# Kernel tuning notes

Hardware: AMD Instinct MI355X
Metric: run time of the kernel (lower is better)

## Reference

```python
import jax, jax.numpy as jnp
import numpy as np

N, E = 50000, 800000
IN_F, OUT_F, EMB, KER = 64, 64, 3, 4


def setup_inputs() -> dict:
    key = jax.random.key(0)
    ks = jax.random.split(key, 6)
    x = jax.random.normal(ks[0], (N, IN_F), dtype=jnp.float32)
    edge_idx = jax.random.randint(ks[1], (2, E), 0, N, dtype=jnp.int64)
    spec_domain = jax.random.normal(ks[2], (N, EMB), dtype=jnp.float32)
    weight = 0.1 * jax.random.normal(ks[3], (IN_F, OUT_F, KER), dtype=jnp.float32)
    bias_p = 0.1 * jax.random.normal(ks[4], (OUT_F,), dtype=jnp.float32)
    mu = 0.005 * jax.random.normal(ks[5], (EMB, KER), dtype=jnp.float32)
    sig = jnp.ones((1, KER), dtype=jnp.float32)  # repo default 60140 underflows exp with random embeddings
    return {"x": x, "edge_idx": edge_idx, "spec_domain": spec_domain,
            "weight": weight, "bias_p": bias_p, "mu": mu, "sig": sig}


def reference(x, edge_idx, spec_domain, weight, bias_p, mu, sig):
    n = x.shape[0]
    row, col = edge_idx[0], edge_idx[1]
    # support for all kernels at once: [N, out, K]
    support = jnp.einsum('ni,iok->nok', x, weight)
    # per-edge Gaussian kernel values: [E, K]
    diff = spec_domain[row] - spec_domain[col]               # [E, emb]
    dm = diff[:, :, None] - mu[None, :, :]                   # [E, emb, K]
    qq = -0.5 * jnp.sum(dm * dm, axis=1)                     # [E, K]
    value = jnp.exp(sig[0][None, :] * qq)                    # [E, K]
    # sparse mm: out[row] += value * support[col], per kernel
    msgs = value[:, None, :] * support[col]                  # [E, out, K]
    out = jax.ops.segment_sum(msgs, row, num_segments=n)     # [N, out, K]
    return out.sum(axis=2) + bias_p
```

## Files before the change

### kernel.cpp

```cpp
#include <hip/hip_runtime.h>
#include <hip/hip_fp16.h>

#define FIN 64
#define CAP 48
#define BINSH 8
#define NBINMAX 256
#define PCAP 5120
#define TILE_B 4096

typedef __attribute__((ext_vector_type(8))) short short8v;
typedef __attribute__((ext_vector_type(4))) float f32x4v;

__device__ __forceinline__ unsigned pk_bf16(float a, float b) {
    unsigned ua = __builtin_bit_cast(unsigned, a);
    unsigned ub = __builtin_bit_cast(unsigned, b);
    ua = (ua + 0x7FFFu + ((ua >> 16) & 1u)) >> 16;
    ub = (ub + 0x7FFFu + ((ub >> 16) & 1u)) >> 16;
    return ua | (ub << 16);
}

__global__ __launch_bounds__(256) void p1_kernel(const float* __restrict__ x,
                                                 const float* __restrict__ weight,
                                                 __half* __restrict__ sup,
                                                 const int* __restrict__ eidx,
                                                 int* __restrict__ gcur,
                                                 int* __restrict__ part,
                                                 int n, int e_total, int sblocks) {
    const int t = threadIdx.x;
    __shared__ unsigned short xb[32][72];
    __shared__ int hist[NBINMAX], lbase[NBINMAX], gbase[NBINMAX];
    __shared__ int wsum[4];

    const int rowbase = blockIdx.x * 32;
    if (rowbase < n) {
        {
            int nrows = n - rowbase; if (nrows > 32) nrows = 32;
            int nf2 = nrows * 32;
            const float2* __restrict__ x2 = (const float2*)(x + (size_t)rowbase * 64);
            #pragma unroll
            for (int j = 0; j < 4; ++j) {
                int idx = t + j * 256;
                if (idx < nf2) {
                    float2 v = x2[idx];
                    int r = idx >> 5, c2 = idx & 31;
                    *(unsigned*)&xb[r][c2 * 2] = pk_bf16(v.x, v.y);
                }
            }
        }
        __syncthreads();

        const int lane = t & 63;
        const int w4 = t >> 6;
        const int lm = lane & 15, lg = lane >> 4;

        short8v a[2][2];
        #pragma unroll
        for (int mt = 0; mt < 2; ++mt)
            #pragma unroll
            for (int kb = 0; kb < 2; ++kb)
                a[mt][kb] = *(const short8v*)&xb[mt * 16 + lm][kb * 32 + lg * 8];

        f32x4v acc[2][4];
        #pragma unroll
        for (int mt = 0; mt < 2; ++mt)
            #pragma unroll
            for (int nt = 0; nt < 4; ++nt)
                acc[mt][nt] = (f32x4v){0.f, 0.f, 0.f, 0.f};

        #pragma unroll
        for (int nt = 0; nt < 4; ++nt) {
            const int col = (w4 * 4 + nt) * 16 + lm;
            short8v bfr[2];
            #pragma unroll
            for (int kb = 0; kb < 2; ++kb) {
                short8v bb;
                #pragma unroll
                for (int j = 0; j < 8; ++j) {
                    float wv = weight[(kb * 32 + lg * 8 + j) * 256 + col];
                    unsigned u = __builtin_bit_cast(unsigned, wv);
                    bb[j] = (short)((u + 0x7FFFu + ((u >> 16) & 1u)) >> 16);
                }
                bfr[kb] = bb;
            }
            #pragma unroll
            for (int mt = 0; mt < 2; ++mt) {
                acc[mt][nt] = __builtin_amdgcn_mfma_f32_16x16x32_bf16(a[mt][0], bfr[0], acc[mt][nt], 0, 0, 0);
                acc[mt][nt] = __builtin_amdgcn_mfma_f32_16x16x32_bf16(a[mt][1], bfr[1], acc[mt][nt], 0, 0, 0);
            }
        }

        #pragma unroll
        for (int mt = 0; mt < 2; ++mt) {
            const int row0 = rowbase + mt * 16 + lg * 4;
            #pragma unroll
            for (int reg = 0; reg < 4; ++reg) {
                if (row0 + reg < n) {
                    #pragma unroll
                    for (int nt = 0; nt < 4; ++nt) {
                        int col = (w4 * 4 + nt) * 16 + lm;
                        sup[(size_t)(row0 + reg) * 256 + col] = __float2half(acc[mt][nt][reg]);
                    }
                }
            }
        }
    }

    if (blockIdx.x < sblocks) {
        int nz = 0;
        #pragma unroll
        for (int j = 1; j < 16; j += 2) nz |= eidx[j];
        const int is64 = (nz == 0);

        hist[t] = 0;
        __syncthreads();

        const int base = blockIdx.x * TILE_B;
        int nv = e_total - base;
        if (nv > TILE_B) nv = TILE_B;
        if (nv < 0) nv = 0;

        int pay[16], bn[16], lp[16];
        #pragma unroll
        for (int i = 0; i < 8; ++i) {
            const int pl = t + 256 * i;
            const int pg = (base >> 1) + pl;
            int r0 = 0, c0 = 0, r1 = 0, c1 = 0, v0 = 0, v1 = 0;
            if (2 * pl < nv) {
                if (is64) {
                    int4 rr = ((const int4*)eidx)[pg];
                    int4 cc = ((const int4*)(eidx + 2 * (size_t)e_total))[pg];
                    r0 = rr.x; c0 = cc.x; v0 = 1;
                    if (2 * pl + 1 < nv) { r1 = rr.z; c1 = cc.z; v1 = 1; }
                } else {
                    int2 rr = ((const int2*)eidx)[pg];
                    int2 cc = ((const int2*)(eidx + (size_t)e_total))[pg];
                    r0 = rr.x; c0 = cc.x; v0 = 1;
                    if (2 * pl + 1 < nv) { r1 = rr.y; c1 = cc.y; v1 = 1; }
                }
            }
            pay[2 * i]     = (c0 << 8) | (r0 & 255);
            bn[2 * i]      = v0 ? (r0 >> BINSH) : -1;
            pay[2 * i + 1] = (c1 << 8) | (r1 & 255);
            bn[2 * i + 1]  = v1 ? (r1 >> BINSH) : -1;
        }
        #pragma unroll
        for (int i = 0; i < 16; ++i) {
            lp[i] = (bn[i] >= 0) ? atomicAdd(&hist[bn[i]], 1) : 0;
        }
        __syncthreads();

        {
            const int lane = t & 63;
            const int w = t >> 6;
            int h = hist[t];
            int s = h;
            #pragma unroll
            for (int off = 1; off < 64; off <<= 1) {
                int u = __shfl_up(s, off, 64);
                if (lane >= off) s += u;
            }
            if (lane == 63) wsum[w] = s;
            __syncthreads();
            if (t == 0) {
                int a0 = 0;
                #pragma unroll
                for (int q = 0; q < 4; ++q) { int u = wsum[q]; wsum[q] = a0; a0 += u; }
            }
            __syncthreads();
            lbase[t] = s - h + wsum[w];
            gbase[t] = (h > 0) ? atomicAdd(&gcur[t], h) : 0;
        }
        __syncthreads();

        #pragma unroll
        for (int i = 0; i < 16; ++i) {
            if (bn[i] >= 0) {
                int dst = gbase[bn[i]] + lp[i];
                if (dst < PCAP) part[bn[i] * PCAP + dst] = pay[i];
            }
        }
    }
}

__global__ __launch_bounds__(1024) void p2_kernel(const int* __restrict__ gcur,
                                                  const int* __restrict__ part,
                                                  const float* __restrict__ spec,
                                                  const float* __restrict__ mu,
                                                  const float* __restrict__ sig,
                                                  int* __restrict__ cnt,
                                                  int* __restrict__ scol,
                                                  uint2* __restrict__ sval, int n) {
    __shared__ int cl[256];
    const int t = threadIdx.x;
    const int b = blockIdx.x;
    const int row0 = b << BINSH;
    if (t < 256) cl[t] = 0;
    __syncthreads();

    float m0[4], m1[4], m2[4], sg[4];
    #pragma unroll
    for (int k = 0; k < 4; ++k) {
        m0[k] = mu[k]; m1[k] = mu[4 + k]; m2[k] = mu[8 + k]; sg[k] = sig[k];
    }

    int nloc = gcur[b];
    if (nloc > PCAP) nloc = PCAP;
    const int* __restrict__ mypart = part + b * PCAP;

    for (int i = t; i < nloc; i += 1024) {
        int e = mypart[i];
        int rl = e & 255;
        int col = ((unsigned)e) >> 8;
        int row = row0 + rl;

        float d0 = spec[row * 3 + 0] - spec[col * 3 + 0];
        float d1 = spec[row * 3 + 1] - spec[col * 3 + 1];
        float d2 = spec[row * 3 + 2] - spec[col * 3 + 2];
        float v[4];
        #pragma unroll
        for (int k = 0; k < 4; ++k) {
            float a = d0 - m0[k], bb = d1 - m1[k], c = d2 - m2[k];
            v[k] = __expf(sg[k] * (-0.5f * (a * a + bb * bb + c * c)));
        }
        union { __half2 h; unsigned u; } p01, p23;
        p01.h = __floats2half2_rn(v[0], v[1]);
        p23.h = __floats2half2_rn(v[2], v[3]);

        int pos = atomicAdd(&cl[rl], 1);
        if (pos < CAP) {
            scol[(size_t)row * CAP + pos] = col;
            sval[(size_t)row * CAP + pos] = make_uint2(p01.u, p23.u);
        }
    }
    __syncthreads();

    int row = row0 + t;
    if (t < 256 && row < n) cnt[row] = (cl[t] > CAP) ? CAP : cl[t];
}

__device__ __forceinline__ float dot_supv(uint2 p, uint2 pv) {
    float2 f0 = __half22float2(__builtin_bit_cast(__half2, p.x));
    float2 f1 = __half22float2(__builtin_bit_cast(__half2, p.y));
    float2 a0 = __half22float2(__builtin_bit_cast(__half2, pv.x));
    float2 a1 = __half22float2(__builtin_bit_cast(__half2, pv.y));
    return f0.x * a0.x + f0.y * a0.y + f1.x * a1.x + f1.y * a1.y;
}

__global__ __launch_bounds__(256, 6) void row_kernel(const int* __restrict__ cnt,
                                                     const int* __restrict__ scol,
                                                     const uint2* __restrict__ sval,
                                                     const __half* __restrict__ sup,
                                                     const float* __restrict__ bias,
                                                     float* __restrict__ out, int n) {
    const int lane = threadIdx.x & 63;
    const int wl = threadIdx.x >> 6;
    const int wv = __builtin_amdgcn_readfirstlane(blockIdx.x * 4 + wl);
    const int NW = gridDim.x * 4;
    const float bias_l = bias[lane];
    const unsigned un = (unsigned)n;

    for (int r = wv; r < n; r += NW) {
        int ec = cnt[r];
        if (ec > CAP) ec = CAP;
        const size_t base = (size_t)r * CAP;
        float acc = bias_l;

        for (int j = 0; j < ec; j += 16) {
            int c[16]; uint2 w[16];
            #pragma unroll
            for (int i = 0; i < 16; ++i) {
                int idx = j + i;
                int cc = scol[base + idx];
                uint2 ww = sval[base + idx];
                bool valid = idx < ec;
                c[i] = ((unsigned)cc < un) ? cc : 0;
                w[i] = valid ? ww : make_uint2(0u, 0u);
            }
            uint2 p[16];
            #pragma unroll
            for (int i = 0; i < 16; ++i)
                p[i] = *(const uint2*)(sup + ((size_t)c[i] * 256 + lane * 4));
            #pragma unroll
            for (int i = 0; i < 16; ++i)
                acc += dot_supv(p[i], w[i]);
        }
        out[(size_t)r * 64 + lane] = acc;
    }
}

extern "C" void kernel_launch(void* const* d_in, const int* in_sizes, int n_in,
                              void* d_out, int out_size, void* d_ws, size_t ws_size,
                              hipStream_t stream) {
    const float* x      = (const float*)d_in[0];
    const int*   eidx   = (const int*)d_in[1];
    const float* spec   = (const float*)d_in[2];
    const float* weight = (const float*)d_in[3];
    const float* bias   = (const float*)d_in[4];
    const float* mu     = (const float*)d_in[5];
    const float* sig    = (const float*)d_in[6];
    float* out = (float*)d_out;

    const int N = in_sizes[0] / FIN;
    const int E = in_sizes[1] / 2;
    const int NB32 = (N + 31) / 32;
    const int SBLK = (E + TILE_B - 1) / TILE_B;
    const int NBIN = (N + (1 << BINSH) - 1) >> BINSH;

    char* w = (char*)d_ws;
    size_t off = 0;
    int* gcur = (int*)(w + off);            off += NBINMAX * 4;
    __half* sup = (__half*)(w + off);       off += (size_t)N * 256 * sizeof(__half);
    off = (off + 255) & ~(size_t)255;
    int* cnt = (int*)(w + off);             off += (size_t)N * 4;
    off = (off + 255) & ~(size_t)255;
    int* scol = (int*)(w + off);            off += (size_t)N * CAP * 4;
    off = (off + 255) & ~(size_t)255;
    uint2* sval = (uint2*)(w + off);        off += (size_t)N * CAP * 8;
    off = (off + 255) & ~(size_t)255;
    int* part = (int*)(w + off);            off += (size_t)NBIN * PCAP * 4;

    hipMemsetAsync(gcur, 0, NBINMAX * 4, stream);
    p1_kernel<<<NB32, 256, 0, stream>>>(x, weight, sup, eidx, gcur, part, N, E, SBLK);
    p2_kernel<<<NBIN, 1024, 0, stream>>>(gcur, part, spec, mu, sig, cnt, scol, sval, N);
    row_kernel<<<1536, 256, 0, stream>>>(cnt, scol, sval, sup, bias, out, N);
}
```

Baseline: 105.0 us.

## Double binning tile size and reload edge indices instead of holding payloads in registers

Each scatter block now bins 8192 edges instead of 4096, so half as many blocks run and global cursor atomics are paid half as often. To keep register pressure manageable, the first pass reads only row indices to build the histogram. A second pass reloads both row and column indices to compute and write payloads, in place of keeping pay/bn arrays in registers. The trade-off is a second read of the row index stream and fewer, longer blocks, which can reduce parallelism in this phase.

```diff
diff --git a/kernel.cpp b/kernel.cpp
--- a/kernel.cpp
+++ b/kernel.cpp
@@ -6,7 +6,7 @@
 #define BINSH 8
 #define NBINMAX 256
 #define PCAP 5120
-#define TILE_B 4096
+#define TILE_B 8192
 
 typedef __attribute__((ext_vector_type(8))) short short8v;
 typedef __attribute__((ext_vector_type(4))) float f32x4v;
@@ -119,9 +119,53 @@
         if (nv > TILE_B) nv = TILE_B;
         if (nv < 0) nv = 0;
 
-        int pay[16], bn[16], lp[16];
-        #pragma unroll
-        for (int i = 0; i < 8; ++i) {
+        int lp[32];
+        #pragma unroll
+        for (int i = 0; i < 16; ++i) {
+            const int pl = t + 256 * i;
+            const int pg = (base >> 1) + pl;
+            int r0 = 0, r1 = 0, v0 = 0, v1 = 0;
+            if (2 * pl < nv) {
+                if (is64) {
+                    int4 rr = ((const int4*)eidx)[pg];
+                    r0 = rr.x; v0 = 1;
+                    if (2 * pl + 1 < nv) { r1 = rr.z; v1 = 1; }
+                } else {
+                    int2 rr = ((const int2*)eidx)[pg];
+                    r0 = rr.x; v0 = 1;
+                    if (2 * pl + 1 < nv) { r1 = rr.y; v1 = 1; }
+                }
+            }
+            lp[2 * i]     = v0 ? atomicAdd(&hist[r0 >> BINSH], 1) : 0;
+            lp[2 * i + 1] = v1 ? atomicAdd(&hist[r1 >> BINSH], 1) : 0;
+        }
+        __syncthreads();
+
+        {
+            const int lane = t & 63;
+            const int w = t >> 6;
+            int h = hist[t];
+            int s = h;
+            #pragma unroll
+            for (int off = 1; off < 64; off <<= 1) {
+                int u = __shfl_up(s, off, 64);
+                if (lane >= off) s += u;
+            }
+            if (lane == 63) wsum[w] = s;
+            __syncthreads();
+            if (t == 0) {
+                int a0 = 0;
+                #pragma unroll
+                for (int q = 0; q < 4; ++q) { int u = wsum[q]; wsum[q] = a0; a0 += u; }
+            }
+            __syncthreads();
+            lbase[t] = s - h + wsum[w];
+            gbase[t] = (h > 0) ? atomicAdd(&gcur[t], h) : 0;
+        }
+        __syncthreads();
+
+        #pragma unroll
+        for (int i = 0; i < 16; ++i) {
             const int pl = t + 256 * i;
             const int pg = (base >> 1) + pl;
             int r0 = 0, c0 = 0, r1 = 0, c1 = 0, v0 = 0, v1 = 0;
@@ -138,45 +182,15 @@
                     if (2 * pl + 1 < nv) { r1 = rr.y; c1 = cc.y; v1 = 1; }
                 }
             }
-            pay[2 * i]     = (c0 << 8) | (r0 & 255);
-            bn[2 * i]      = v0 ? (r0 >> BINSH) : -1;
-            pay[2 * i + 1] = (c1 << 8) | (r1 & 255);
-            bn[2 * i + 1]  = v1 ? (r1 >> BINSH) : -1;
-        }
-        #pragma unroll
-        for (int i = 0; i < 16; ++i) {
-            lp[i] = (bn[i] >= 0) ? atomicAdd(&hist[bn[i]], 1) : 0;
-        }
-        __syncthreads();
-
-        {
-            const int lane = t & 63;
-            const int w = t >> 6;
-            int h = hist[t];
-            int s = h;
-            #pragma unroll
-            for (int off = 1; off < 64; off <<= 1) {
-                int u = __shfl_up(s, off, 64);
-                if (lane >= off) s += u;
-            }
-            if (lane == 63) wsum[w] = s;
-            __syncthreads();
-            if (t == 0) {
-                int a0 = 0;
-                #pragma unroll
-                for (int q = 0; q < 4; ++q) { int u = wsum[q]; wsum[q] = a0; a0 += u; }
-            }
-            __syncthreads();
-            lbase[t] = s - h + wsum[w];
-            gbase[t] = (h > 0) ? atomicAdd(&gcur[t], h) : 0;
-        }
-        __syncthreads();
-
-        #pragma unroll
-        for (int i = 0; i < 16; ++i) {
-            if (bn[i] >= 0) {
-                int dst = gbase[bn[i]] + lp[i];
-                if (dst < PCAP) part[bn[i] * PCAP + dst] = pay[i];
+            if (v0) {
+                int b = r0 >> BINSH;
+                int dst = gbase[b] + lp[2 * i];
+                if (dst < PCAP) part[b * PCAP + dst] = (c0 << 8) | (r0 & 255);
+            }
+            if (v1) {
+                int b = r1 >> BINSH;
+                int dst = gbase[b] + lp[2 * i + 1];
+                if (dst < PCAP) part[b * PCAP + dst] = (c1 << 8) | (r1 & 255);
             }
         }
     }
```

After: 111.9 us. +6.6%, slower.
